# Kernel tuning notes

Measured on AMD Instinct MI355X. Metric: run time of the kernel, lower is better.

Reference implementation:

```python
import jax, jax.numpy as jnp
import numpy as np

B, T, DIM, S, DFF = 4, 2048, 2048, 4, 8192
SINKHORN_ITERS = 10


def setup_inputs() -> dict:
    key = jax.random.key(0)
    ks = jax.random.split(key, 12)

    def lin(k, fan_in, shape):
        bound = 1.0 / np.sqrt(fan_in)
        return jax.random.uniform(k, shape, jnp.float32, -bound, bound)

    return {
        "x": jax.random.normal(ks[0], (B, T, DIM), jnp.float32),
        # phi_* linears act on the S-times tiled vector of size S*DIM
        "phi_pre_w": lin(ks[1], S * DIM, (S, S * DIM)),
        "phi_pre_b": lin(ks[2], S * DIM, (S,)),
        "phi_post_w": lin(ks[3], S * DIM, (S, S * DIM)),
        "phi_post_b": lin(ks[4], S * DIM, (S,)),
        "phi_res_w": lin(ks[5], S * DIM, (S * S, S * DIM)),
        "phi_res_b": lin(ks[6], S * DIM, (S * S,)),
        "alpha_pre": jnp.ones((1,), jnp.float32),
        "alpha_post": jnp.ones((1,), jnp.float32),
        "alpha_res": jnp.ones((1,), jnp.float32),
        "b_pre": jnp.zeros((S,), jnp.float32),
        "b_post": jnp.zeros((S,), jnp.float32),
        "b_res": jnp.zeros((S, S), jnp.float32),
        # block = transformer MLP
        "W1": lin(ks[7], DIM, (DIM, DFF)),
        "b1": lin(ks[8], DIM, (DFF,)),
        "W2": lin(ks[9], DFF, (DFF, DIM)),
        "b2": lin(ks[10], DFF, (DIM,)),
    }


def sinkhorn_knopp(logits):
    # logits: [B, T, S, S] -> doubly-stochastic via exp + alternating normalization
    M = jnp.exp(logits)
    for _ in range(SINKHORN_ITERS):
        M = M / jnp.sum(M, axis=-1, keepdims=True)  # rows
        M = M / jnp.sum(M, axis=-2, keepdims=True)  # cols
    return M


def reference(x, phi_pre_w, phi_pre_b, phi_post_w, phi_post_b, phi_res_w,
              phi_res_b, alpha_pre, alpha_post, alpha_res, b_pre, b_post,
              b_res, W1, b1, W2, b2):
    bs, seq, d = x.shape
    s = b_pre.shape[0]
    eps = jnp.asarray(jnp.finfo(x.dtype).eps, x.dtype)
    # x_l = x expanded over S identical streams; x_vec = tile(x, S).
    # RMS over the tiled S*d vector == RMS over d (streams are copies).
    x_n = x * jax.lax.rsqrt(jnp.mean(x * x, axis=-1, keepdims=True) + eps)
    # Linear on the tiled vector == sum of the S weight blocks applied to x_n.
    Wp = phi_pre_w.reshape(s, s, d).sum(axis=1)        # [S, d]
    Wq = phi_post_w.reshape(s, s, d).sum(axis=1)       # [S, d]
    Wr = phi_res_w.reshape(s * s, s, d).sum(axis=1)    # [S*S, d]
    h_pre_t = alpha_pre * (jnp.einsum('btd,sd->bts', x_n, Wp) + phi_pre_b) + b_pre
    h_post_t = alpha_post * (jnp.einsum('btd,sd->bts', x_n, Wq) + phi_post_b) + b_post
    h_res_t = alpha_res * (jnp.einsum('btd,kd->btk', x_n, Wr) + phi_res_b)
    h_res_t = h_res_t.reshape(bs, seq, s, s) + b_res
    h_pre = jax.nn.sigmoid(h_pre_t)                    # [B,T,S]
    h_post = 2.0 * jax.nn.sigmoid(h_post_t)            # [B,T,S]
    h_res = sinkhorn_knopp(h_res_t)                    # [B,T,S,S]
    # block_input = sum_j x_l[:,:,j] * h_pre[...,j] ; streams identical -> x * sum_j h_pre
    block_input = x * jnp.sum(h_pre, axis=-1, keepdims=True)
    # block: MLP with exact (erf) GELU, matching torch default
    h = jax.nn.gelu(jnp.einsum('btd,df->btf', block_input, W1) + b1, approximate=False)
    block_out = jnp.einsum('btf,fd->btd', h, W2) + b2
    # out = sum_i [ (h_res @ x_l)_i + h_post_i * block_out ]
    #     = x * sum_{ij} h_res[ij] + block_out * sum_i h_post_i
    res_mix = jnp.sum(h_res, axis=(-2, -1))[..., None]         # [B,T,1]
    post_mix = jnp.sum(h_post, axis=-1, keepdims=True)          # [B,T,1]
    return x * res_mix + block_out * post_mix
```

## Files before the change

kernel.cpp:

```cpp
#include <hip/hip_runtime.h>
#include <hip/hip_bf16.h>
#include <cstdint>
#include <cstddef>

#define DIM   2048
#define DFF   8192
#define NROWS 8192
#define NFOLD 24

typedef float f32x4 __attribute__((ext_vector_type(4)));
typedef __bf16 bf16x8 __attribute__((ext_vector_type(8)));

__device__ __forceinline__ float sigmoidf_(float v) { return 1.0f / (1.0f + expf(-v)); }

__device__ __forceinline__ unsigned short f2bf(float v) {
    union { __hip_bfloat16 h; unsigned short u; } cv;
    cv.h = __float2bfloat16(v);
    return cv.u;
}

__device__ __forceinline__ void async_copy16(const void* g, void* l) {
    __builtin_amdgcn_global_load_lds((const __attribute__((address_space(1))) void*)g,
                                     (__attribute__((address_space(3))) void*)l, 16, 0, 0);
}

__device__ __forceinline__ void wg_barrier() {
    asm volatile("" ::: "memory");
    __builtin_amdgcn_s_barrier();
    asm volatile("" ::: "memory");
}

__global__ __launch_bounds__(256) void fold_kernel(const float* __restrict__ pre_w,
                                                   const float* __restrict__ post_w,
                                                   const float* __restrict__ res_w,
                                                   float* __restrict__ Wfold) {
    int idx = blockIdx.x * 256 + threadIdx.x;
    if (idx >= NFOLD * DIM) return;
    int r = idx >> 11;
    int d = idx & (DIM - 1);
    const float* src;
    if (r < 4)      src = pre_w  + (size_t)r * (4 * DIM);
    else if (r < 8) src = post_w + (size_t)(r - 4) * (4 * DIM);
    else            src = res_w  + (size_t)(r - 8) * (4 * DIM);
    Wfold[idx] = src[d] + src[DIM + d] + src[2 * DIM + d] + src[3 * DIM + d];
}

__global__ __launch_bounds__(256) void transpose_to_bf16(const float* __restrict__ in,
                                                         __hip_bfloat16* __restrict__ out,
                                                         int R, int C) {
    __shared__ float tile[32][33];
    int bx = blockIdx.x, by = blockIdx.y;
    int tx = threadIdx.x & 31, ty0 = threadIdx.x >> 5;
#pragma unroll
    for (int i = 0; i < 4; i++) {
        int ty = ty0 + i * 8;
        tile[ty][tx] = in[(size_t)(by * 32 + ty) * C + bx * 32 + tx];
    }
    __syncthreads();
#pragma unroll
    for (int i = 0; i < 4; i++) {
        int ty = ty0 + i * 8;
        out[(size_t)(bx * 32 + ty) * R + by * 32 + tx] = __float2bfloat16(tile[tx][ty]);
    }
}

__global__ __launch_bounds__(512) void gating_kernel(
    const float* __restrict__ x, const float* __restrict__ Wfold,
    const float* __restrict__ phi_pre_b, const float* __restrict__ phi_post_b,
    const float* __restrict__ phi_res_b,
    const float* __restrict__ alpha_pre, const float* __restrict__ alpha_post,
    const float* __restrict__ alpha_res,
    const float* __restrict__ b_pre, const float* __restrict__ b_post,
    const float* __restrict__ b_res,
    __hip_bfloat16* __restrict__ Abuf,
    float* __restrict__ g_res_arr, float* __restrict__ g_post_arr) {
    const int tid = threadIdx.x;
    const int lane = tid & 63, wave = tid >> 6;
    const int row = blockIdx.x * 8 + wave;

    const float4* x4 = (const float4*)x + (size_t)row * 512;
    const float4* w4 = (const float4*)Wfold;

    float4 xv[8];
#pragma unroll
    for (int j = 0; j < 8; j++) xv[j] = x4[j * 64 + lane];

    float p[25];
    p[24] = 0.f;
#pragma unroll
    for (int j = 0; j < 8; j++)
        p[24] += xv[j].x * xv[j].x + xv[j].y * xv[j].y + xv[j].z * xv[j].z + xv[j].w * xv[j].w;

    for (int r = 0; r < NFOLD; r++) {
        float acc = 0.f;
#pragma unroll
        for (int j = 0; j < 8; j++) {
            float4 wv = w4[r * 512 + j * 64 + lane];
            acc += xv[j].x * wv.x + xv[j].y * wv.y + xv[j].z * wv.z + xv[j].w * wv.w;
        }
        p[r] = acc;
    }

#pragma unroll
    for (int r = 0; r < 25; r++) {
        float v = p[r];
#pragma unroll
        for (int off = 1; off < 64; off <<= 1) v += __shfl_xor(v, off, 64);
        p[r] = v;
    }

    const float rms = rsqrtf(p[24] / (float)DIM + 1.1920928955078125e-07f);
    const float ap = alpha_pre[0], aq = alpha_post[0], ar = alpha_res[0];
    float gpre = 0.f, gpost = 0.f;
#pragma unroll
    for (int s = 0; s < 4; s++) {
        gpre  += sigmoidf_(ap * (rms * p[s]     + phi_pre_b[s])  + b_pre[s]);
        gpost += 2.0f * sigmoidf_(aq * (rms * p[4 + s] + phi_post_b[s]) + b_post[s]);
    }
    float Mm[4][4];
#pragma unroll
    for (int i = 0; i < 4; i++)
#pragma unroll
        for (int j = 0; j < 4; j++) {
            int k = i * 4 + j;
            Mm[i][j] = expf(ar * (rms * p[8 + k] + phi_res_b[k]) + b_res[k]);
        }
    for (int it = 0; it < 10; ++it) {
#pragma unroll
        for (int i = 0; i < 4; i++) {
            float rs = 1.0f / (Mm[i][0] + Mm[i][1] + Mm[i][2] + Mm[i][3]);
#pragma unroll
            for (int j = 0; j < 4; j++) Mm[i][j] *= rs;
        }
#pragma unroll
        for (int j = 0; j < 4; j++) {
            float cs = 1.0f / (Mm[0][j] + Mm[1][j] + Mm[2][j] + Mm[3][j]);
#pragma unroll
            for (int i = 0; i < 4; i++) Mm[i][j] *= cs;
        }
    }
    float gres = 0.f;
#pragma unroll
    for (int i = 0; i < 4; i++)
#pragma unroll
        for (int j = 0; j < 4; j++) gres += Mm[i][j];

    __hip_bfloat16* arow = Abuf + (size_t)row * DIM;
#pragma unroll
    for (int j = 0; j < 8; j++) {
        ushort4 u;
        u.x = f2bf(xv[j].x * gpre); u.y = f2bf(xv[j].y * gpre);
        u.z = f2bf(xv[j].z * gpre); u.w = f2bf(xv[j].w * gpre);
        *reinterpret_cast<ushort4*>(arow + (j * 64 + lane) * 4) = u;
    }
    if (lane == 0) {
        g_res_arr[row]  = gres;
        g_post_arr[row] = gpost;
    }
}

#define RDA(DST, SRC, mh)                                                        \
    _Pragma("unroll") for (int m = 0; m < 4; ++m) {                              \
        DST[m][0] = *(const bf16x8*)((SRC) + baseA + ((mh) * 4 + m) * 2048 + cb0); \
        DST[m][1] = *(const bf16x8*)((SRC) + baseA + ((mh) * 4 + m) * 2048 + cb1); \
    }

#define RDB(DST, SRC, nh)                                                        \
    _Pragma("unroll") for (int n = 0; n < 2; ++n) {                              \
        DST[n][0] = *(const bf16x8*)((SRC) + baseB + ((nh) * 2 + n) * 2048 + cb0); \
        DST[n][1] = *(const bf16x8*)((SRC) + baseB + ((nh) * 2 + n) * 2048 + cb1); \
    }

#define MQP(AREG, BREG, mh, nh)                                                  \
    __builtin_amdgcn_s_setprio(1);                                               \
    _Pragma("unroll") for (int m = 0; m < 4; ++m)                                \
    _Pragma("unroll") for (int n = 0; n < 2; ++n) {                              \
        acc[(mh)*4+m][(nh)*2+n] = __builtin_amdgcn_mfma_f32_16x16x32_bf16(       \
            AREG[m][0], BREG[n][0], acc[(mh)*4+m][(nh)*2+n], 0, 0, 0);           \
        acc[(mh)*4+m][(nh)*2+n] = __builtin_amdgcn_mfma_f32_16x16x32_bf16(       \
            AREG[m][1], BREG[n][1], acc[(mh)*4+m][(nh)*2+n], 0, 0, 0);           \
    }                                                                            \
    __builtin_amdgcn_s_setprio(0);

#define STG(matb, srcArr, ldsb, t_, h_)                                          \
    if ((t_) < nk) {                                                             \
        char* l_ = (ldsb) + (((t_) & 1) * 32768) + (h_) * 16384 + wave * 1024;   \
        async_copy16((matb) + (size_t)srcArr[0][h_] + (size_t)(t_) * 128, l_);   \
        async_copy16((matb) + (size_t)srcArr[1][h_] + (size_t)(t_) * 128, l_ + 8192); \
    }

template <int MODE, int NTLOG>
__global__ __launch_bounds__(512, 2) void gemm256(
    const __hip_bfloat16* __restrict__ A, const __hip_bfloat16* __restrict__ Bt,
    int M, int N, int K, const float* __restrict__ bias,
    __hip_bfloat16* __restrict__ outh, float* __restrict__ outf,
    const float* __restrict__ x, const float* __restrict__ g_res,
    const float* __restrict__ g_post) {
    __shared__ __align__(16) char ldsA[65536];
    __shared__ __align__(16) char ldsB[65536];

    const int nwg = gridDim.x;
    const int wg = blockIdx.x;
    const int swz = (wg & 7) * (nwg >> 3) + (wg >> 3);
    const int mt = swz >> NTLOG;
    const int nt = swz & ((1 << NTLOG) - 1);
    const int m0 = mt * 256;
    const int n0 = nt * 256;

    const int tid = threadIdx.x;
    const int lane = tid & 63;
    const int wave = tid >> 6;
    const int wr = wave >> 2;
    const int wc = wave & 3;
    const int q = lane >> 4;
    const int rr = lane & 7;

    const uint32_t cb0 = (uint32_t)((q ^ rr) << 4);
    const uint32_t cb1 = (uint32_t)(((4 + q) ^ rr) << 4);
    const uint32_t baseA = (uint32_t)((wr * 128 + (lane & 15)) * 128);
    const uint32_t baseB = (uint32_t)((wc * 64 + (lane & 15)) * 128);

    const int srow = wave * 8 + (lane >> 3);
    const uint32_t scb = (uint32_t)((((lane & 7) ^ ((lane >> 3) & 7))) << 4);
    uint32_t aSrc[2][2], bSrc[2][2];
#pragma unroll
    for (int i = 0; i < 2; ++i)
#pragma unroll
        for (int h = 0; h < 2; ++h) {
            aSrc[i][h] = (uint32_t)(m0 + h * 128 + i * 64 + srow) * (uint32_t)(K * 2) + scb;
            bSrc[i][h] = (uint32_t)(n0 + h * 128 + i * 64 + srow) * (uint32_t)(K * 2) + scb;
        }
    const char* Ab = (const char*)A;
    const char* Bb = (const char*)Bt;

    f32x4 acc[8][4];
#pragma unroll
    for (int m = 0; m < 8; ++m)
#pragma unroll
        for (int n = 0; n < 4; ++n) acc[m][n] = (f32x4){0.f, 0.f, 0.f, 0.f};

    const int nk = K / 64;

    STG(Ab, aSrc, ldsA, 0, 0) STG(Ab, aSrc, ldsA, 0, 1)
    STG(Bb, bSrc, ldsB, 0, 0) STG(Bb, bSrc, ldsB, 0, 1)
    STG(Bb, bSrc, ldsB, 1, 0) STG(Bb, bSrc, ldsB, 1, 1)
    asm volatile("s_waitcnt vmcnt(4)" ::: "memory");
    wg_barrier();

    bf16x8 a0[4][2], a1[4][2];
    bf16x8 b0[2][2], b1[2][2];
    RDA(a0, ldsA, 0)
    RDB(b0, ldsB, 0)

    for (int kt = 0; kt < nk; ++kt) {
        const char* sA  = ldsA + (kt & 1) * 32768;
        const char* sB  = ldsB + (kt & 1) * 32768;
        const char* sAn = ldsA + ((kt + 1) & 1) * 32768;
        const char* sBn = ldsB + ((kt + 1) & 1) * 32768;
        RDB(b1, sB, 1)
        STG(Ab, aSrc, ldsA, kt + 1, 0)
        wg_barrier();
        MQP(a0, b0, 0, 0)
        wg_barrier();
        RDA(a1, sA, 1)
        STG(Ab, aSrc, ldsA, kt + 1, 1)
        wg_barrier();
        MQP(a0, b1, 0, 1)
        wg_barrier();
        STG(Bb, bSrc, ldsB, kt + 2, 0)
        wg_barrier();
        MQP(a1, b0, 1, 0)
        wg_barrier();
        STG(Bb, bSrc, ldsB, kt + 2, 1)
        if (kt + 2 < nk) {
            asm volatile("s_waitcnt vmcnt(4)" ::: "memory");
        } else if (kt + 1 < nk) {
            asm volatile("s_waitcnt vmcnt(0)" ::: "memory");
        }
        wg_barrier();
        if (kt + 1 < nk) {
            RDA(a0, sAn, 0)
            RDB(b0, sBn, 0)
        }
        MQP(a1, b1, 1, 1)
    }

    const int crow0 = m0 + wr * 128;
    const int ccol0 = n0 + wc * 64;
#pragma unroll
    for (int mi = 0; mi < 8; ++mi) {
#pragma unroll
        for (int ni = 0; ni < 4; ++ni) {
            const int col = ccol0 + ni * 16 + (lane & 15);
            const float bc = bias[col];
#pragma unroll
            for (int j = 0; j < 4; ++j) {
                const int row = crow0 + mi * 16 + q * 4 + j;
                float v = acc[mi][ni][j] + bc;
                if (MODE == 1) {
                    float u = 1.5957691216057308f * (v + 0.044715f * v * v * v);
                    float s = 1.0f / (1.0f + __expf(-u));
                    outh[(size_t)row * N + col] = __float2bfloat16(v * s);
                } else {
                    outf[(size_t)row * N + col] =
                        x[(size_t)row * N + col] * g_res[row] + v * g_post[row];
                }
            }
        }
    }
}

extern "C" void kernel_launch(void* const* d_in, const int* in_sizes, int n_in,
                              void* d_out, int out_size, void* d_ws, size_t ws_size,
                              hipStream_t stream) {
    const float* x          = (const float*)d_in[0];
    const float* phi_pre_w  = (const float*)d_in[1];
    const float* phi_pre_b  = (const float*)d_in[2];
    const float* phi_post_w = (const float*)d_in[3];
    const float* phi_post_b = (const float*)d_in[4];
    const float* phi_res_w  = (const float*)d_in[5];
    const float* phi_res_b  = (const float*)d_in[6];
    const float* alpha_pre  = (const float*)d_in[7];
    const float* alpha_post = (const float*)d_in[8];
    const float* alpha_res  = (const float*)d_in[9];
    const float* b_pre      = (const float*)d_in[10];
    const float* b_post     = (const float*)d_in[11];
    const float* b_res      = (const float*)d_in[12];
    const float* W1         = (const float*)d_in[13];
    const float* b1         = (const float*)d_in[14];
    const float* W2         = (const float*)d_in[15];
    const float* b2         = (const float*)d_in[16];
    float* out = (float*)d_out;

    char* ws = (char*)d_ws;
    __hip_bfloat16* W1T  = (__hip_bfloat16*)ws;
    __hip_bfloat16* W2T  = W1T + (size_t)DFF * DIM;
    __hip_bfloat16* Abuf = W2T + (size_t)DIM * DFF;
    __hip_bfloat16* Hbuf = Abuf + (size_t)NROWS * DIM;
    float* Wfold = (float*)(Hbuf + (size_t)NROWS * DFF);
    float* gres  = Wfold + NFOLD * DIM;
    float* gpost = gres + NROWS;

    fold_kernel<<<(NFOLD * DIM + 255) / 256, 256, 0, stream>>>(phi_pre_w, phi_post_w,
                                                               phi_res_w, Wfold);
    transpose_to_bf16<<<dim3(DFF / 32, DIM / 32), 256, 0, stream>>>(W1, W1T, DIM, DFF);
    transpose_to_bf16<<<dim3(DIM / 32, DFF / 32), 256, 0, stream>>>(W2, W2T, DFF, DIM);
    gating_kernel<<<NROWS / 8, 512, 0, stream>>>(x, Wfold, phi_pre_b, phi_post_b, phi_res_b,
                                                 alpha_pre, alpha_post, alpha_res,
                                                 b_pre, b_post, b_res, Abuf, gres, gpost);
    gemm256<1, 5><<<1024, 512, 0, stream>>>(
        Abuf, W1T, NROWS, DFF, DIM, b1, Hbuf, nullptr, nullptr, nullptr, nullptr);
    gemm256<2, 3><<<256, 512, 0, stream>>>(
        Hbuf, W2T, NROWS, DIM, DFF, b2, nullptr, out, x, gres, gpost);
}
```

Measured before the change: 762.1 us.

## Restructure GEMM pipeline with quadrant LDS layout and XCD-aware tile mapping

```diff
diff --git a/kernel.cpp b/kernel.cpp
--- a/kernel.cpp
+++ b/kernel.cpp
@@ -29,6 +29,9 @@
     __builtin_amdgcn_s_barrier();
     asm volatile("" ::: "memory");
 }
+
+#define VM(n) asm volatile("s_waitcnt vmcnt(" #n ")" ::: "memory")
+#define LGKM0 asm volatile("s_waitcnt lgkmcnt(0)" ::: "memory")
 
 __global__ __launch_bounds__(256) void fold_kernel(const float* __restrict__ pre_w,
                                                    const float* __restrict__ post_w,
@@ -159,37 +162,52 @@
     }
 }
 
-#define RDA(DST, SRC, mh)                                                        \
-    _Pragma("unroll") for (int m = 0; m < 4; ++m) {                              \
-        DST[m][0] = *(const bf16x8*)((SRC) + baseA + ((mh) * 4 + m) * 2048 + cb0); \
-        DST[m][1] = *(const bf16x8*)((SRC) + baseA + ((mh) * 4 + m) * 2048 + cb1); \
-    }
-
-#define RDB(DST, SRC, nh)                                                        \
-    _Pragma("unroll") for (int n = 0; n < 2; ++n) {                              \
-        DST[n][0] = *(const bf16x8*)((SRC) + baseB + ((nh) * 2 + n) * 2048 + cb0); \
-        DST[n][1] = *(const bf16x8*)((SRC) + baseB + ((nh) * 2 + n) * 2048 + cb1); \
-    }
-
-#define MQP(AREG, BREG, mh, nh)                                                  \
-    __builtin_amdgcn_s_setprio(1);                                               \
-    _Pragma("unroll") for (int m = 0; m < 4; ++m)                                \
-    _Pragma("unroll") for (int n = 0; n < 2; ++n) {                              \
-        acc[(mh)*4+m][(nh)*2+n] = __builtin_amdgcn_mfma_f32_16x16x32_bf16(       \
-            AREG[m][0], BREG[n][0], acc[(mh)*4+m][(nh)*2+n], 0, 0, 0);           \
-        acc[(mh)*4+m][(nh)*2+n] = __builtin_amdgcn_mfma_f32_16x16x32_bf16(       \
-            AREG[m][1], BREG[n][1], acc[(mh)*4+m][(nh)*2+n], 0, 0, 0);           \
-    }                                                                            \
+#define RD_A0                                                                     \
+    _Pragma("unroll") for (int m = 0; m < 4; ++m) {                               \
+        a0[m][0] = *(const bf16x8*)(A0r + baseA + m * 2048 + cb0);                \
+        a0[m][1] = *(const bf16x8*)(A0r + baseA + m * 2048 + cb1);                \
+    }
+#define RD_A1                                                                     \
+    _Pragma("unroll") for (int m = 0; m < 4; ++m) {                               \
+        a1[m][0] = *(const bf16x8*)(A1r + baseA + m * 2048 + cb0);                \
+        a1[m][1] = *(const bf16x8*)(A1r + baseA + m * 2048 + cb1);                \
+    }
+#define RD_B0                                                                     \
+    _Pragma("unroll") for (int n = 0; n < 2; ++n) {                               \
+        b0[n][0] = *(const bf16x8*)(B0r + baseB + n * 2048 + cb0);                \
+        b0[n][1] = *(const bf16x8*)(B0r + baseB + n * 2048 + cb1);                \
+    }
+#define RD_B1                                                                     \
+    _Pragma("unroll") for (int n = 0; n < 2; ++n) {                               \
+        b1[n][0] = *(const bf16x8*)(B1r + baseB + n * 2048 + cb0);                \
+        b1[n][1] = *(const bf16x8*)(B1r + baseB + n * 2048 + cb1);                \
+    }
+
+#define MQ(AF, BF, MO, NO)                                                        \
+    __builtin_amdgcn_s_setprio(1);                                                \
+    _Pragma("unroll") for (int m = 0; m < 4; ++m)                                 \
+    _Pragma("unroll") for (int n = 0; n < 2; ++n) {                               \
+        acc[(MO) + m][(NO) + n] = __builtin_amdgcn_mfma_f32_16x16x32_bf16(        \
+            AF[m][0], BF[n][0], acc[(MO) + m][(NO) + n], 0, 0, 0);                \
+        acc[(MO) + m][(NO) + n] = __builtin_amdgcn_mfma_f32_16x16x32_bf16(        \
+            AF[m][1], BF[n][1], acc[(MO) + m][(NO) + n], 0, 0, 0);                \
+    }                                                                             \
     __builtin_amdgcn_s_setprio(0);
 
-#define STG(matb, srcArr, ldsb, t_, h_)                                          \
-    if ((t_) < nk) {                                                             \
-        char* l_ = (ldsb) + (((t_) & 1) * 32768) + (h_) * 16384 + wave * 1024;   \
-        async_copy16((matb) + (size_t)srcArr[0][h_] + (size_t)(t_) * 128, l_);   \
-        async_copy16((matb) + (size_t)srcArr[1][h_] + (size_t)(t_) * 128, l_ + 8192); \
-    }
-
-template <int MODE, int NTLOG>
+#define STG_A(t_, h_)                                                             \
+    if ((t_) < nk) {                                                              \
+        char* l_ = ldsA + (((t_) & 1) * 32768) + (h_) * 16384 + wave * 1024;      \
+        async_copy16(Ab + aOff[0][h_] + (size_t)(t_) * 128, l_);                  \
+        async_copy16(Ab + aOff[1][h_] + (size_t)(t_) * 128, l_ + 8192);           \
+    }
+#define STG_B(t_, h_)                                                             \
+    if ((t_) < nk) {                                                              \
+        char* l_ = ldsB + (((t_) & 1) * 32768) + (h_) * 16384 + wave * 1024;      \
+        async_copy16(Bb + bOff[0][h_] + (size_t)(t_) * 128, l_);                  \
+        async_copy16(Bb + bOff[1][h_] + (size_t)(t_) * 128, l_ + 8192);           \
+    }
+
+template <int MODE, int NB>
 __global__ __launch_bounds__(512, 2) void gemm256(
     const __hip_bfloat16* __restrict__ A, const __hip_bfloat16* __restrict__ Bt,
     int M, int N, int K, const float* __restrict__ bias,
@@ -199,11 +217,11 @@
     __shared__ __align__(16) char ldsA[65536];
     __shared__ __align__(16) char ldsB[65536];
 
-    const int nwg = gridDim.x;
     const int wg = blockIdx.x;
-    const int swz = (wg & 7) * (nwg >> 3) + (wg >> 3);
-    const int mt = swz >> NTLOG;
-    const int nt = swz & ((1 << NTLOG) - 1);
+    const int xcd = wg & 7;
+    const int i = wg >> 3;
+    const int nt = xcd * NB + (i % NB);
+    const int mt = i / NB;
     const int m0 = mt * 256;
     const int n0 = nt * 256;
 
@@ -217,18 +235,21 @@
 
     const uint32_t cb0 = (uint32_t)((q ^ rr) << 4);
     const uint32_t cb1 = (uint32_t)(((4 + q) ^ rr) << 4);
-    const uint32_t baseA = (uint32_t)((wr * 128 + (lane & 15)) * 128);
-    const uint32_t baseB = (uint32_t)((wc * 64 + (lane & 15)) * 128);
-
-    const int srow = wave * 8 + (lane >> 3);
+    const uint32_t baseA = (uint32_t)((wr * 64 + (lane & 15)) * 128);
+    const uint32_t baseB = (uint32_t)((wc * 32 + (lane & 15)) * 128);
+
     const uint32_t scb = (uint32_t)((((lane & 7) ^ ((lane >> 3) & 7))) << 4);
-    uint32_t aSrc[2][2], bSrc[2][2];
-#pragma unroll
-    for (int i = 0; i < 2; ++i)
+    const int lr = lane >> 3;
+    const size_t K2 = (size_t)K * 2;
+    size_t aOff[2][2], bOff[2][2];
+#pragma unroll
+    for (int ii = 0; ii < 2; ++ii)
 #pragma unroll
         for (int h = 0; h < 2; ++h) {
-            aSrc[i][h] = (uint32_t)(m0 + h * 128 + i * 64 + srow) * (uint32_t)(K * 2) + scb;
-            bSrc[i][h] = (uint32_t)(n0 + h * 128 + i * 64 + srow) * (uint32_t)(K * 2) + scb;
+            int gA = m0 + wave * 8 + lr + ii * 128 + h * 64;
+            int gB = n0 + ((wave >> 2) + 2 * ii) * 64 + h * 32 + (wave & 3) * 8 + lr;
+            aOff[ii][h] = (size_t)gA * K2 + scb;
+            bOff[ii][h] = (size_t)gB * K2 + scb;
         }
     const char* Ab = (const char*)A;
     const char* Bb = (const char*)Bt;
@@ -241,61 +262,60 @@
 
     const int nk = K / 64;
 
-    STG(Ab, aSrc, ldsA, 0, 0) STG(Ab, aSrc, ldsA, 0, 1)
-    STG(Bb, bSrc, ldsB, 0, 0) STG(Bb, bSrc, ldsB, 0, 1)
-    STG(Bb, bSrc, ldsB, 1, 0) STG(Bb, bSrc, ldsB, 1, 1)
-    asm volatile("s_waitcnt vmcnt(4)" ::: "memory");
+    STG_A(0, 0); STG_B(0, 0); STG_B(0, 1); STG_A(0, 1);
+    STG_A(1, 0); STG_B(1, 0); STG_B(1, 1); STG_A(1, 1);
+    VM(12);
     wg_barrier();
 
     bf16x8 a0[4][2], a1[4][2];
     bf16x8 b0[2][2], b1[2][2];
-    RDA(a0, ldsA, 0)
-    RDB(b0, ldsB, 0)
 
     for (int kt = 0; kt < nk; ++kt) {
-        const char* sA  = ldsA + (kt & 1) * 32768;
-        const char* sB  = ldsB + (kt & 1) * 32768;
-        const char* sAn = ldsA + ((kt + 1) & 1) * 32768;
-        const char* sBn = ldsB + ((kt + 1) & 1) * 32768;
-        RDB(b1, sB, 1)
-        STG(Ab, aSrc, ldsA, kt + 1, 0)
-        wg_barrier();
-        MQP(a0, b0, 0, 0)
-        wg_barrier();
-        RDA(a1, sA, 1)
-        STG(Ab, aSrc, ldsA, kt + 1, 1)
-        wg_barrier();
-        MQP(a0, b1, 0, 1)
-        wg_barrier();
-        STG(Bb, bSrc, ldsB, kt + 2, 0)
-        wg_barrier();
-        MQP(a1, b0, 1, 0)
-        wg_barrier();
-        STG(Bb, bSrc, ldsB, kt + 2, 1)
+        const int c = kt & 1;
+        const char* A0r = ldsA + c * 32768;
+        const char* A1r = A0r + 16384;
+        const char* B0r = ldsB + c * 32768;
+        const char* B1r = B0r + 16384;
+        RD_A0
+        RD_B0
+        if (kt + 1 < nk) { VM(10); } else { VM(2); }
+        wg_barrier();
+        MQ(a0, b0, 0, 0)
+        LGKM0;
+        wg_barrier();
+        RD_B1
+        STG_A(kt + 2, 0); STG_B(kt + 2, 0);
+        if (kt + 2 < nk) { VM(12); } else if (kt + 1 < nk) { VM(8); } else { VM(0); }
+        wg_barrier();
+        MQ(a0, b1, 0, 2)
+        LGKM0;
+        wg_barrier();
+        RD_A1
+        STG_B(kt + 2, 1);
+        wg_barrier();
+        MQ(a1, b0, 4, 0)
+        LGKM0;
+        wg_barrier();
+        STG_A(kt + 2, 1);
         if (kt + 2 < nk) {
-            asm volatile("s_waitcnt vmcnt(4)" ::: "memory");
+            VM(12);
+            wg_barrier();
         } else if (kt + 1 < nk) {
-            asm volatile("s_waitcnt vmcnt(0)" ::: "memory");
-        }
-        wg_barrier();
-        if (kt + 1 < nk) {
-            RDA(a0, sAn, 0)
-            RDB(b0, sBn, 0)
-        }
-        MQP(a1, b1, 1, 1)
-    }
-
-    const int crow0 = m0 + wr * 128;
-    const int ccol0 = n0 + wc * 64;
+            VM(4);
+            wg_barrier();
+        }
+        MQ(a1, b1, 4, 2)
+    }
+
 #pragma unroll
     for (int mi = 0; mi < 8; ++mi) {
 #pragma unroll
         for (int ni = 0; ni < 4; ++ni) {
-            const int col = ccol0 + ni * 16 + (lane & 15);
+            const int col = n0 + wc * 64 + (ni >> 1) * 32 + (ni & 1) * 16 + (lane & 15);
             const float bc = bias[col];
 #pragma unroll
             for (int j = 0; j < 4; ++j) {
-                const int row = crow0 + mi * 16 + q * 4 + j;
+                const int row = m0 + wr * 128 + (mi >> 2) * 64 + (mi & 3) * 16 + q * 4 + j;
                 float v = acc[mi][ni][j] + bc;
                 if (MODE == 1) {
                     float u = 1.5957691216057308f * (v + 0.044715f * v * v * v);
@@ -348,8 +368,8 @@
     gating_kernel<<<NROWS / 8, 512, 0, stream>>>(x, Wfold, phi_pre_b, phi_post_b, phi_res_b,
                                                  alpha_pre, alpha_post, alpha_res,
                                                  b_pre, b_post, b_res, Abuf, gres, gpost);
-    gemm256<1, 5><<<1024, 512, 0, stream>>>(
+    gemm256<1, 4><<<1024, 512, 0, stream>>>(
         Abuf, W1T, NROWS, DFF, DIM, b1, Hbuf, nullptr, nullptr, nullptr, nullptr);
-    gemm256<2, 3><<<256, 512, 0, stream>>>(
+    gemm256<2, 1><<<256, 512, 0, stream>>>(
         Hbuf, W2T, NROWS, DIM, DFF, b2, nullptr, out, x, gres, gpost);
 }
```

New measurement: 721.1 us. 1.06x faster.
